# Optimization experiments

Measured on AMD Instinct MI355X. Metric: run time of the kernel, lower is better.

Reference implementation:

```python
import jax, jax.numpy as jnp
import numpy as np

N = 50000       # nodes
E = 800000      # edges (before self-loops)
F_IN = 128      # in_channels
HID = 32        # hidden_channels per head
HEADS = 4
OUT = 16        # out_channels
NEG_SLOPE = 0.2 # PyG GATConv leaky_relu slope
EPS = 1e-16     # PyG softmax denominator eps
BN_EPS = 1e-5


def setup_inputs() -> dict:
    key = jax.random.key(0)
    ks = jax.random.split(key, 20)
    rn = lambda k, shp, s=0.1: (jax.random.normal(k, shp, jnp.float32) * s)
    x = jax.random.normal(ks[0], (N, F_IN), jnp.float32)
    edge_index = jax.random.randint(ks[1], (2, E), 0, N, dtype=jnp.int32)
    D0 = HEADS * HID  # 128
    return {
        "x": x, "edge_index": edge_index,
        # layer 0: GATConv(F_IN -> HID, heads=HEADS, concat=True)
        "W0": rn(ks[2], (F_IN, HEADS * HID)), "as0": rn(ks[3], (HEADS, HID)),
        "ad0": rn(ks[4], (HEADS, HID)), "b0": jnp.zeros((D0,), jnp.float32),
        "g0": jnp.ones((D0,), jnp.float32) + rn(ks[5], (D0,), 0.05),
        "be0": rn(ks[6], (D0,), 0.05),
        # layer 1: GATConv(D0 -> HID, heads=HEADS, concat=True)
        "W1": rn(ks[7], (D0, HEADS * HID)), "as1": rn(ks[8], (HEADS, HID)),
        "ad1": rn(ks[9], (HEADS, HID)), "b1": jnp.zeros((D0,), jnp.float32),
        "g1": jnp.ones((D0,), jnp.float32) + rn(ks[10], (D0,), 0.05),
        "be1": rn(ks[11], (D0,), 0.05),
        # layer 2: GATConv(D0 -> OUT, heads=1, concat=False)
        "W2": rn(ks[12], (D0, OUT)), "as2": rn(ks[13], (1, OUT)),
        "ad2": rn(ks[14], (1, OUT)), "b2": jnp.zeros((OUT,), jnp.float32),
    }


def _gat(x, src, dst, W, a_s, a_d, b, heads, ch, concat):
    n = x.shape[0]
    h = (x @ W).reshape(n, heads, ch)                       # [N,H,C]
    score_s = (h * a_s).sum(-1)                             # [N,H]
    score_d = (h * a_d).sum(-1)                             # [N,H]
    e = jax.nn.leaky_relu(score_s[src] + score_d[dst], NEG_SLOPE)  # [E,H]
    emax = jax.ops.segment_max(e, dst, num_segments=n)
    emax = jnp.where(jnp.isfinite(emax), emax, 0.0)
    p = jnp.exp(e - emax[dst])
    denom = jax.ops.segment_sum(p, dst, num_segments=n)
    alpha = p / (denom[dst] + EPS)                          # segment softmax over dst
    out = jax.ops.segment_sum(h[src] * alpha[:, :, None], dst, num_segments=n)
    out = out.reshape(n, heads * ch) if concat else out.mean(axis=1)
    return out + b


def _bn(x, g, be):
    m = x.mean(0)
    v = x.var(0)
    return (x - m) * jax.lax.rsqrt(v + BN_EPS) * g + be


def reference(x, edge_index, W0, as0, ad0, b0, g0, be0,
              W1, as1, ad1, b1, g1, be1, W2, as2, ad2, b2):
    n = x.shape[0]
    loop = jnp.arange(n, dtype=edge_index.dtype)
    src = jnp.concatenate([edge_index[0], loop])  # PyG add_self_loops
    dst = jnp.concatenate([edge_index[1], loop])
    h = _gat(x, src, dst, W0, as0, ad0, b0, HEADS, HID, True)
    h = jax.nn.elu(_bn(h, g0, be0))                 # dropout disabled (eval)
    h = _gat(h, src, dst, W1, as1, ad1, b1, HEADS, HID, True)
    h = jax.nn.elu(_bn(h, g1, be1))
    return _gat(h, src, dst, W2, as2, ad2, b2, 1, OUT, False)
```

## Files before the change

kernel.cpp:

```cpp
#include <hip/hip_runtime.h>
#include <hip/hip_bf16.h>
#include <math.h>

#define NEG_SLOPE 0.2f
#define EPS_SM 1e-16f
#define BN_EPS 1e-5f
#define RANK_BLOCKS 512

typedef __attribute__((ext_vector_type(8))) short bf16x8;
typedef __attribute__((ext_vector_type(4))) float f32x4;

__device__ __forceinline__ float lrelu(float x) { return x > 0.f ? x : NEG_SLOPE * x; }
__device__ __forceinline__ ushort f2bf(float f) {
    uint u = __float_as_uint(f);
    return (ushort)((u + 0x7FFFu + ((u >> 16) & 1u)) >> 16);
}
__device__ __forceinline__ float bfl(uint u) { return __uint_as_float(u << 16); }
__device__ __forceinline__ float bfh(uint u) { return __uint_as_float(u & 0xFFFF0000u); }

__global__ void pack_w(const float* __restrict__ W0, const float* __restrict__ W1,
                       const float* __restrict__ W2, ushort* __restrict__ P0,
                       ushort* __restrict__ P1, ushort* __restrict__ P2) {
    int i = blockIdx.x * blockDim.x + threadIdx.x;
    const float* W;
    ushort* P;
    int NC, s;
    if (i < 16384) { W = W0; P = P0; NC = 128; s = i; }
    else if (i < 32768) { W = W1; P = P1; NC = 128; s = i - 16384; }
    else if (i < 34816) { W = W2; P = P2; NC = 16; s = i - 32768; }
    else return;
    int k = s / NC, col = s % NC;
    int CT = NC >> 4;
    int dst = (((k >> 5) * CT + (col >> 4)) << 9) +
              (((col & 15) | (((k >> 3) & 3) << 4)) << 3) + (k & 7);
    P[dst] = f2bf(W[s]);
}

template <int NC, int HEADS, bool XBN, bool RANKFUSE>
__global__ __launch_bounds__(256) void gemm_mfma(
    const void* __restrict__ Xv, const ushort* __restrict__ Wp, ushort* __restrict__ Hb,
    int n, const float* __restrict__ sumsP, const float* __restrict__ g,
    const float* __restrict__ be, const float* __restrict__ as_, const float* __restrict__ ad_,
    float* __restrict__ ss, float* __restrict__ sd,
    const int* __restrict__ dstE, int E, int* __restrict__ deg, ushort* __restrict__ rank) {
    int tid = threadIdx.x;
    if constexpr (RANKFUSE) {
        if ((int)blockIdx.x < RANK_BLOCKS) {
            int T = RANK_BLOCKS * 256;
            for (int i = (int)blockIdx.x * 256 + tid; i < E; i += T)
                rank[i] = (ushort)atomicAdd(&deg[dstE[i]], 1);
            return;
        }
    }
    constexpr int CT = NC / 16;
    constexpr int FPH = NC / HEADS / 16;
    __shared__ __align__(16) ushort Xb[64 * 128];
    __shared__ float ssl[64 * HEADS], sdl[64 * HEADS];
    int bid = RANKFUSE ? ((int)blockIdx.x - RANK_BLOCKS) : (int)blockIdx.x;
    int row0 = bid * 64;
    if constexpr (!XBN) {
        const float* X = (const float*)Xv;
#pragma unroll
        for (int i = 0; i < 8; ++i) {
            int idx = tid + i * 256;
            int row = idx >> 5, q = idx & 31;
            int gr = row0 + row;
            float4 v = make_float4(0.f, 0.f, 0.f, 0.f);
            if (gr < n) v = ((const float4*)(X + (long)gr * 128))[q];
            ushort4 p = make_ushort4(f2bf(v.x), f2bf(v.y), f2bf(v.z), f2bf(v.w));
            int s = (q >> 1) ^ (row & 15);
            *(ushort4*)&Xb[row * 128 + s * 8 + (q & 1) * 4] = p;
        }
    } else {
        const ushort* X = (const ushort*)Xv;
        int c8 = (tid & 15) * 8;
        float inv_n = 1.f / (float)n;
        float bm[8], bs[8], bb[8];
#pragma unroll
        for (int j = 0; j < 8; ++j) {
            int ch = c8 + j;
            float m = sumsP[ch * 16] * inv_n;
            float vv = fmaxf(sumsP[(128 + ch) * 16] * inv_n - m * m, 0.f);
            bm[j] = m;
            bs[j] = rsqrtf(vv + BN_EPS) * g[ch];
            bb[j] = be[ch];
        }
#pragma unroll
        for (int i = 0; i < 4; ++i) {
            int idx = tid + i * 256;
            int row = idx >> 4, g8 = idx & 15;
            int gr = row0 + row;
            uint4 v = make_uint4(0, 0, 0, 0);
            if (gr < n) v = ((const uint4*)(X + (long)gr * 128))[g8];
            float a, b;
#define BNE(comp, j0)                                                  \
    a = bfl(comp); b = bfh(comp);                                      \
    a = (a - bm[j0]) * bs[j0] + bb[j0]; a = a > 0.f ? a : expm1f(a);   \
    b = (b - bm[j0 + 1]) * bs[j0 + 1] + bb[j0 + 1];                    \
    b = b > 0.f ? b : expm1f(b);                                       \
    comp = (uint)f2bf(a) | ((uint)f2bf(b) << 16);
            BNE(v.x, 0) BNE(v.y, 2) BNE(v.z, 4) BNE(v.w, 6)
#undef BNE
            int s = g8 ^ (row & 15);
            *(uint4*)&Xb[row * 128 + s * 8] = v;
        }
    }
    __syncthreads();
    int lane = tid & 63;
    int w = tid >> 6;
    int r0 = w * 16;
    int lrow = lane & 15, lhi = lane >> 4;
    f32x4 zero = {0.f, 0.f, 0.f, 0.f};
    f32x4 acc[CT];
#pragma unroll
    for (int f = 0; f < CT; ++f) acc[f] = zero;
    const ushort* xr = &Xb[(r0 + lrow) * 128];
#pragma unroll
    for (int ks = 0; ks < 4; ++ks) {
        int kg = ks * 4 + lhi;
        bf16x8 a = *(const bf16x8*)&xr[(kg ^ lrow) << 3];
#pragma unroll
        for (int f = 0; f < CT; ++f) {
            bf16x8 b = *(const bf16x8*)&Wp[((ks * CT + f) * 64 + lane) * 8];
            acc[f] = __builtin_amdgcn_mfma_f32_16x16x32_bf16(a, b, acc[f], 0, 0, 0);
        }
    }
    __syncthreads();
#pragma unroll
    for (int f = 0; f < CT; ++f)
#pragma unroll
        for (int j = 0; j < 4; ++j)
            Xb[(r0 + lhi * 4 + j) * NC + f * 16 + lrow] = f2bf(acc[f][j]);
    float asv[CT], adv[CT];
#pragma unroll
    for (int f = 0; f < CT; ++f) {
        asv[f] = as_[f * 16 + lrow];
        adv[f] = ad_[f * 16 + lrow];
    }
#pragma unroll
    for (int h = 0; h < HEADS; ++h) {
        float ps[4] = {}, pd[4] = {};
#pragma unroll
        for (int fi = 0; fi < FPH; ++fi) {
            int f = h * FPH + fi;
#pragma unroll
            for (int j = 0; j < 4; ++j) {
                ps[j] = fmaf(acc[f][j], asv[f], ps[j]);
                pd[j] = fmaf(acc[f][j], adv[f], pd[j]);
            }
        }
#pragma unroll
        for (int j = 0; j < 4; ++j) {
#pragma unroll
            for (int d = 1; d < 16; d <<= 1) {
                ps[j] += __shfl_xor(ps[j], d, 64);
                pd[j] += __shfl_xor(pd[j], d, 64);
            }
            if (lrow == 0) {
                ssl[(r0 + lhi * 4 + j) * HEADS + h] = ps[j];
                sdl[(r0 + lhi * 4 + j) * HEADS + h] = pd[j];
            }
        }
    }
    __syncthreads();
    constexpr int NU = 64 * NC / 8;
#pragma unroll
    for (int i = 0; i < (NU + 255) / 256; ++i) {
        int idx = tid + i * 256;
        if (idx < NU) {
            int row = idx / (NC / 8), c8i = idx % (NC / 8);
            int gr = row0 + row;
            if (gr < n) ((uint4*)&Hb[(long)gr * NC])[c8i] = ((const uint4*)Xb)[idx];
        }
    }
    if (tid < 64 * HEADS) {
        int row = tid / HEADS, hh = tid % HEADS;
        int gr = row0 + row;
        if (gr < n) {
            ss[(long)gr * HEADS + hh] = ssl[tid];
            sd[(long)gr * HEADS + hh] = sdl[tid];
        }
    }
}

__global__ __launch_bounds__(1024) void scan_kernel(const int* __restrict__ deg,
                                                    int* __restrict__ offs, int n) {
    __shared__ int wsum[16];
    __shared__ int wpre[16];
    __shared__ int carry_s;
    int tid = threadIdx.x;
    int lane = tid & 63;
    int w = tid >> 6;
    if (tid == 0) carry_s = 0;
    __syncthreads();
    int nv = (n + 3) >> 2;
    for (int base = 0; base < nv; base += 1024) {
        int carry = carry_s;
        int gi = base + tid;
        int e0 = gi * 4;
        int4 v = make_int4(0, 0, 0, 0);
        if (e0 + 3 < n) {
            v = ((const int4*)deg)[gi];
        } else if (e0 < n) {
            v.x = deg[e0];
            if (e0 + 1 < n) v.y = deg[e0 + 1];
            if (e0 + 2 < n) v.z = deg[e0 + 2];
        }
        int tsum = v.x + v.y + v.z + v.w;
        int incl = tsum;
#pragma unroll
        for (int d = 1; d < 64; d <<= 1) {
            int t = __shfl_up(incl, d, 64);
            if (lane >= d) incl += t;
        }
        if (lane == 63) wsum[w] = incl;
        __syncthreads();
        if (w == 0 && lane < 16) {
            int s = wsum[lane];
#pragma unroll
            for (int d = 1; d < 16; d <<= 1) {
                int t = __shfl_up(s, d, 64);
                if (lane >= d) s += t;
            }
            wpre[lane] = s;
        }
        __syncthreads();
        int wbase = (w == 0) ? 0 : wpre[w - 1];
        int ex = carry + wbase + incl - tsum;
        if (e0 < n) {
            int4 o;
            o.x = ex;
            o.y = ex + v.x;
            o.z = o.y + v.y;
            o.w = o.z + v.z;
            if (e0 + 3 < n) {
                ((int4*)offs)[gi] = o;
            } else {
                offs[e0] = o.x;
                if (e0 + 1 < n) offs[e0 + 1] = o.y;
                if (e0 + 2 < n) offs[e0 + 2] = o.z;
            }
        }
        __syncthreads();
        if (tid == 1023) carry_s = carry + wpre[15];
        __syncthreads();
    }
}

__global__ void scatter_kernel(const int* __restrict__ src, const int* __restrict__ dst,
                               const ushort* __restrict__ rank, const int* __restrict__ offs,
                               int E, int* __restrict__ srcs) {
    int i = blockIdx.x * blockDim.x + threadIdx.x;
    int T = gridDim.x * blockDim.x;
    for (; i < E; i += T) {
        int d = dst[i];
        srcs[offs[d] + (int)rank[i]] = src[i];
    }
}

__global__ __launch_bounds__(256) void gat_gather4(
    const uint* __restrict__ hb, const float* __restrict__ ss, const float* __restrict__ sd,
    const int* __restrict__ offs, const int* __restrict__ deg, const int* __restrict__ srcs,
    const float* __restrict__ bias, ushort* __restrict__ outb, int n) {
    int wid = threadIdx.x >> 6;
    int lane = threadIdx.x & 63;
    int node = blockIdx.x * 4 + wid;
    if (node >= n) return;
    int off = offs[node];
    int dg = deg[node];
    int grp = lane >> 4;
    int ll = lane & 15;
    int hd = ll >> 2;
    float sdn = sd[node * 4 + hd];
    float es = lrelu(ss[node * 4 + hd] + sdn);
    const uint* hrow = hb + ll * 4;
    float acc[8] = {};
    float sm = 0.f;
#pragma unroll 2
    for (int i = grp; i < dg; i += 4) {
        int s = srcs[off + i];
        float w = __expf(lrelu(ss[s * 4 + hd] + sdn));
        sm += w;
        uint4 hv = *(const uint4*)(hrow + (long)s * 64);
        acc[0] = fmaf(w, bfl(hv.x), acc[0]);
        acc[1] = fmaf(w, bfh(hv.x), acc[1]);
        acc[2] = fmaf(w, bfl(hv.y), acc[2]);
        acc[3] = fmaf(w, bfh(hv.y), acc[3]);
        acc[4] = fmaf(w, bfl(hv.z), acc[4]);
        acc[5] = fmaf(w, bfh(hv.z), acc[5]);
        acc[6] = fmaf(w, bfl(hv.w), acc[6]);
        acc[7] = fmaf(w, bfh(hv.w), acc[7]);
    }
#pragma unroll
    for (int j = 0; j < 8; ++j) {
        acc[j] += __shfl_xor(acc[j], 16, 64);
        acc[j] += __shfl_xor(acc[j], 32, 64);
    }
    sm += __shfl_xor(sm, 16, 64);
    sm += __shfl_xor(sm, 32, 64);
    float wS = __expf(es);
    sm += wS;
    uint4 hvS = *(const uint4*)(hrow + (long)node * 64);
    acc[0] = fmaf(wS, bfl(hvS.x), acc[0]);
    acc[1] = fmaf(wS, bfh(hvS.x), acc[1]);
    acc[2] = fmaf(wS, bfl(hvS.y), acc[2]);
    acc[3] = fmaf(wS, bfh(hvS.y), acc[3]);
    acc[4] = fmaf(wS, bfl(hvS.z), acc[4]);
    acc[5] = fmaf(wS, bfh(hvS.z), acc[5]);
    acc[6] = fmaf(wS, bfl(hvS.w), acc[6]);
    acc[7] = fmaf(wS, bfh(hvS.w), acc[7]);
    float inv = 1.f / (sm + EPS_SM);
    if (grp == 0) {
        float4 bA = *(const float4*)&bias[ll * 8];
        float4 bB = *(const float4*)&bias[ll * 8 + 4];
        uint4 p;
        p.x = (uint)f2bf(acc[0] * inv + bA.x) | ((uint)f2bf(acc[1] * inv + bA.y) << 16);
        p.y = (uint)f2bf(acc[2] * inv + bA.z) | ((uint)f2bf(acc[3] * inv + bA.w) << 16);
        p.z = (uint)f2bf(acc[4] * inv + bB.x) | ((uint)f2bf(acc[5] * inv + bB.y) << 16);
        p.w = (uint)f2bf(acc[6] * inv + bB.z) | ((uint)f2bf(acc[7] * inv + bB.w) << 16);
        *(uint4*)&outb[(long)node * 128 + ll * 8] = p;
    }
}

__global__ __launch_bounds__(256) void gat_gather1(
    const uint* __restrict__ hb2, const float* __restrict__ ss, const float* __restrict__ sd,
    const int* __restrict__ offs, const int* __restrict__ deg, const int* __restrict__ srcs,
    const float* __restrict__ bias, float* __restrict__ out, int n) {
    int wid = threadIdx.x >> 6;
    int lane = threadIdx.x & 63;
    int node = blockIdx.x * 4 + wid;
    if (node >= n) return;
    int off = offs[node];
    int dg = deg[node];
    int grp = lane >> 3;
    int ll = lane & 7;
    float sdn = sd[node];
    float es = lrelu(ss[node] + sdn);
    float a0 = 0.f, a1 = 0.f, sm = 0.f;
#pragma unroll 2
    for (int i = grp; i < dg; i += 8) {
        int s = srcs[off + i];
        float w = __expf(lrelu(ss[s] + sdn));
        sm += w;
        uint hv = hb2[s * 8 + ll];
        a0 = fmaf(w, bfl(hv), a0);
        a1 = fmaf(w, bfh(hv), a1);
    }
#pragma unroll
    for (int d = 8; d <= 32; d <<= 1) {
        a0 += __shfl_xor(a0, d, 64);
        a1 += __shfl_xor(a1, d, 64);
        sm += __shfl_xor(sm, d, 64);
    }
    float wS = __expf(es);
    sm += wS;
    uint hvS = hb2[node * 8 + ll];
    a0 = fmaf(wS, bfl(hvS), a0);
    a1 = fmaf(wS, bfh(hvS), a1);
    float inv = 1.f / (sm + EPS_SM);
    if (grp == 0) {
        float2 o = make_float2(a0 * inv + bias[ll * 2], a1 * inv + bias[ll * 2 + 1]);
        *(float2*)&out[(long)node * 16 + ll * 2] = o;
    }
}

__global__ __launch_bounds__(256) void bn_stats_bf16(const uint4* __restrict__ X4,
                                                     float* __restrict__ sumsP, int n) {
    __shared__ float red[4096];
    int tid = threadIdx.x;
    float s[8] = {}, s2[8] = {};
    long tot = (long)n * 16;
    long T = (long)gridDim.x * 256;
    for (long i = (long)blockIdx.x * 256 + tid; i < tot; i += T) {
        uint4 v = X4[i];
        float f;
        f = bfl(v.x); s[0] += f; s2[0] = fmaf(f, f, s2[0]);
        f = bfh(v.x); s[1] += f; s2[1] = fmaf(f, f, s2[1]);
        f = bfl(v.y); s[2] += f; s2[2] = fmaf(f, f, s2[2]);
        f = bfh(v.y); s[3] += f; s2[3] = fmaf(f, f, s2[3]);
        f = bfl(v.z); s[4] += f; s2[4] = fmaf(f, f, s2[4]);
        f = bfh(v.z); s[5] += f; s2[5] = fmaf(f, f, s2[5]);
        f = bfl(v.w); s[6] += f; s2[6] = fmaf(f, f, s2[6]);
        f = bfh(v.w); s[7] += f; s2[7] = fmaf(f, f, s2[7]);
    }
#pragma unroll
    for (int j = 0; j < 8; ++j) {
        red[j * 256 + tid] = s[j];
        red[(8 + j) * 256 + tid] = s2[j];
    }
    __syncthreads();
    int ch = tid & 127, st = tid >> 7;
    int base = (st * 8 + (ch & 7)) * 256 + (ch >> 3);
    float a = 0.f;
#pragma unroll
    for (int rep = 0; rep < 16; ++rep) a += red[base + rep * 16];
    atomicAdd(&sumsP[tid * 16], a);
}

extern "C" void kernel_launch(void* const* d_in, const int* in_sizes, int n_in,
                              void* d_out, int out_size, void* d_ws, size_t ws_size,
                              hipStream_t stream) {
    const float* x = (const float*)d_in[0];
    const int* ei = (const int*)d_in[1];
    const float* W0 = (const float*)d_in[2];
    const float* as0 = (const float*)d_in[3];
    const float* ad0 = (const float*)d_in[4];
    const float* b0 = (const float*)d_in[5];
    const float* g0 = (const float*)d_in[6];
    const float* be0 = (const float*)d_in[7];
    const float* W1 = (const float*)d_in[8];
    const float* as1 = (const float*)d_in[9];
    const float* ad1 = (const float*)d_in[10];
    const float* b1 = (const float*)d_in[11];
    const float* g1 = (const float*)d_in[12];
    const float* be1 = (const float*)d_in[13];
    const float* W2 = (const float*)d_in[14];
    const float* as2 = (const float*)d_in[15];
    const float* ad2 = (const float*)d_in[16];
    const float* b2 = (const float*)d_in[17];

    int n = in_sizes[0] / 128;
    int E = in_sizes[1] / 2;
    const int* srcA = ei;
    const int* dstA = ei + E;

    char* base = (char*)d_ws;
    auto alloc = [&](size_t bytes) {
        char* p = base;
        base += (bytes + 255) & ~(size_t)255;
        return p;
    };
    ushort* hb = (ushort*)alloc((size_t)n * 128 * 2);
    ushort* actb = (ushort*)alloc((size_t)n * 128 * 2);
    ushort* h2b = (ushort*)alloc((size_t)n * 16 * 2);
    float* ssb = (float*)alloc((size_t)n * 4 * 4);
    float* sdb = (float*)alloc((size_t)n * 4 * 4);
    float* sumsP0 = (float*)alloc(4096 * 4);
    float* sumsP1 = (float*)alloc(4096 * 4);
    int* deg = (int*)alloc((size_t)n * 4);
    int* offs = (int*)alloc((size_t)n * 4);
    ushort* rank = (ushort*)alloc((size_t)E * 2);
    int* srcs = (int*)alloc((size_t)E * 4);
    ushort* Wp0 = (ushort*)alloc(16384 * 2);
    ushort* Wp1 = (ushort*)alloc(16384 * 2);
    ushort* Wp2 = (ushort*)alloc(2048 * 2);

    float* out = (float*)d_out;

    hipMemsetAsync(deg, 0, (size_t)n * 4, stream);
    hipMemsetAsync(sumsP0, 0, 4096 * 4 * 2, stream);

    pack_w<<<136, 256, 0, stream>>>(W0, W1, W2, Wp0, Wp1, Wp2);

    int gGemm = (n + 63) / 64;
    int gWave = (n + 3) / 4;

    gemm_mfma<128, 4, false, true><<<RANK_BLOCKS + gGemm, 256, 0, stream>>>(
        x, Wp0, hb, n, nullptr, g0, be0, as0, ad0, ssb, sdb, dstA, E, deg, rank);
    scan_kernel<<<1, 1024, 0, stream>>>(deg, offs, n);
    scatter_kernel<<<2048, 256, 0, stream>>>(srcA, dstA, rank, offs, E, srcs);

    gat_gather4<<<gWave, 256, 0, stream>>>((const uint*)hb, ssb, sdb, offs, deg, srcs, b0, actb, n);
    bn_stats_bf16<<<256, 256, 0, stream>>>((const uint4*)actb, sumsP0, n);

    gemm_mfma<128, 4, true, false><<<gGemm, 256, 0, stream>>>(
        actb, Wp1, hb, n, sumsP0, g0, be0, as1, ad1, ssb, sdb, nullptr, 0, nullptr, nullptr);
    gat_gather4<<<gWave, 256, 0, stream>>>((const uint*)hb, ssb, sdb, offs, deg, srcs, b1, actb, n);
    bn_stats_bf16<<<256, 256, 0, stream>>>((const uint4*)actb, sumsP1, n);

    gemm_mfma<16, 1, true, false><<<gGemm, 256, 0, stream>>>(
        actb, Wp2, h2b, n, sumsP1, g1, be1, as2, ad2, ssb, sdb, nullptr, 0, nullptr, nullptr);
    gat_gather1<<<gWave, 256, 0, stream>>>((const uint*)h2b, ssb, sdb, offs, deg, srcs, b2, out, n);
}
```

Baseline: 242.8 us.

## Pad degree counters to cache lines, unroll rank/scatter loops, derive degree from offsets

Each node's degree counter now sits in its own 64-byte slot, so the atomics that count degrees and assign ranks stop contending on shared cache lines. A small compact kernel then copies the counters into a dense array for the scan. The rank and scatter loops are unrolled four-way so more independent atomics and loads are in flight, and the rank block count is halved. The scan now writes offs[n], so the gather kernels compute degree as offs[node+1]-off instead of reading a separate array, at the cost of one extra kernel launch and a larger counter memset.

```diff
diff --git a/kernel.cpp b/kernel.cpp
--- a/kernel.cpp
+++ b/kernel.cpp
@@ -5,7 +5,7 @@
 #define NEG_SLOPE 0.2f
 #define EPS_SM 1e-16f
 #define BN_EPS 1e-5f
-#define RANK_BLOCKS 512
+#define RANK_BLOCKS 256
 
 typedef __attribute__((ext_vector_type(8))) short bf16x8;
 typedef __attribute__((ext_vector_type(4))) float f32x4;
@@ -42,13 +42,24 @@
     int n, const float* __restrict__ sumsP, const float* __restrict__ g,
     const float* __restrict__ be, const float* __restrict__ as_, const float* __restrict__ ad_,
     float* __restrict__ ss, float* __restrict__ sd,
-    const int* __restrict__ dstE, int E, int* __restrict__ deg, ushort* __restrict__ rank) {
+    const int* __restrict__ dstE, int E, int* __restrict__ degP, ushort* __restrict__ rank) {
     int tid = threadIdx.x;
     if constexpr (RANKFUSE) {
         if ((int)blockIdx.x < RANK_BLOCKS) {
-            int T = RANK_BLOCKS * 256;
-            for (int i = (int)blockIdx.x * 256 + tid; i < E; i += T)
-                rank[i] = (ushort)atomicAdd(&deg[dstE[i]], 1);
+            const int T = RANK_BLOCKS * 256;
+            int i = (int)blockIdx.x * 256 + tid;
+            for (; i + 3 * T < E; i += 4 * T) {
+                int d0 = dstE[i], d1 = dstE[i + T], d2 = dstE[i + 2 * T], d3 = dstE[i + 3 * T];
+                ushort r0 = (ushort)atomicAdd(&degP[d0 << 4], 1);
+                ushort r1 = (ushort)atomicAdd(&degP[d1 << 4], 1);
+                ushort r2 = (ushort)atomicAdd(&degP[d2 << 4], 1);
+                ushort r3 = (ushort)atomicAdd(&degP[d3 << 4], 1);
+                rank[i] = r0;
+                rank[i + T] = r1;
+                rank[i + 2 * T] = r2;
+                rank[i + 3 * T] = r3;
+            }
+            for (; i < E; i += T) rank[i] = (ushort)atomicAdd(&degP[dstE[i] << 4], 1);
             return;
         }
     }
@@ -181,6 +192,11 @@
             sd[(long)gr * HEADS + hh] = sdl[tid];
         }
     }
+}
+
+__global__ void compact_deg(const int* __restrict__ degP, int* __restrict__ deg, int n) {
+    int i = blockIdx.x * blockDim.x + threadIdx.x;
+    if (i < n) deg[i] = degP[i << 4];
 }
 
 __global__ __launch_bounds__(1024) void scan_kernel(const int* __restrict__ deg,
@@ -245,29 +261,38 @@
         if (tid == 1023) carry_s = carry + wpre[15];
         __syncthreads();
     }
+    if (tid == 0) offs[n] = carry_s;
 }
 
 __global__ void scatter_kernel(const int* __restrict__ src, const int* __restrict__ dst,
                                const ushort* __restrict__ rank, const int* __restrict__ offs,
                                int E, int* __restrict__ srcs) {
+    const int T = gridDim.x * blockDim.x;
     int i = blockIdx.x * blockDim.x + threadIdx.x;
-    int T = gridDim.x * blockDim.x;
-    for (; i < E; i += T) {
-        int d = dst[i];
-        srcs[offs[d] + (int)rank[i]] = src[i];
-    }
+    for (; i + 3 * T < E; i += 4 * T) {
+        int d0 = dst[i], d1 = dst[i + T], d2 = dst[i + 2 * T], d3 = dst[i + 3 * T];
+        int p0 = offs[d0] + (int)rank[i];
+        int p1 = offs[d1] + (int)rank[i + T];
+        int p2 = offs[d2] + (int)rank[i + 2 * T];
+        int p3 = offs[d3] + (int)rank[i + 3 * T];
+        srcs[p0] = src[i];
+        srcs[p1] = src[i + T];
+        srcs[p2] = src[i + 2 * T];
+        srcs[p3] = src[i + 3 * T];
+    }
+    for (; i < E; i += T) srcs[offs[dst[i]] + (int)rank[i]] = src[i];
 }
 
 __global__ __launch_bounds__(256) void gat_gather4(
     const uint* __restrict__ hb, const float* __restrict__ ss, const float* __restrict__ sd,
-    const int* __restrict__ offs, const int* __restrict__ deg, const int* __restrict__ srcs,
+    const int* __restrict__ offs, const int* __restrict__ srcs,
     const float* __restrict__ bias, ushort* __restrict__ outb, int n) {
     int wid = threadIdx.x >> 6;
     int lane = threadIdx.x & 63;
     int node = blockIdx.x * 4 + wid;
     if (node >= n) return;
     int off = offs[node];
-    int dg = deg[node];
+    int dg = offs[node + 1] - off;
     int grp = lane >> 4;
     int ll = lane & 15;
     int hd = ll >> 2;
@@ -324,14 +349,14 @@
 
 __global__ __launch_bounds__(256) void gat_gather1(
     const uint* __restrict__ hb2, const float* __restrict__ ss, const float* __restrict__ sd,
-    const int* __restrict__ offs, const int* __restrict__ deg, const int* __restrict__ srcs,
+    const int* __restrict__ offs, const int* __restrict__ srcs,
     const float* __restrict__ bias, float* __restrict__ out, int n) {
     int wid = threadIdx.x >> 6;
     int lane = threadIdx.x & 63;
     int node = blockIdx.x * 4 + wid;
     if (node >= n) return;
     int off = offs[node];
-    int dg = deg[node];
+    int dg = offs[node + 1] - off;
     int grp = lane >> 3;
     int ll = lane & 7;
     float sdn = sd[node];
@@ -437,8 +462,9 @@
     float* sdb = (float*)alloc((size_t)n * 4 * 4);
     float* sumsP0 = (float*)alloc(4096 * 4);
     float* sumsP1 = (float*)alloc(4096 * 4);
+    int* degP = (int*)alloc((size_t)n * 64);
     int* deg = (int*)alloc((size_t)n * 4);
-    int* offs = (int*)alloc((size_t)n * 4);
+    int* offs = (int*)alloc(((size_t)n + 1) * 4);
     ushort* rank = (ushort*)alloc((size_t)E * 2);
     int* srcs = (int*)alloc((size_t)E * 4);
     ushort* Wp0 = (ushort*)alloc(16384 * 2);
@@ -447,28 +473,30 @@
 
     float* out = (float*)d_out;
 
-    hipMemsetAsync(deg, 0, (size_t)n * 4, stream);
+    hipMemsetAsync(degP, 0, (size_t)n * 64, stream);
     hipMemsetAsync(sumsP0, 0, 4096 * 4 * 2, stream);
 
     pack_w<<<136, 256, 0, stream>>>(W0, W1, W2, Wp0, Wp1, Wp2);
 
     int gGemm = (n + 63) / 64;
     int gWave = (n + 3) / 4;
+    int gNode = (n + 255) / 256;
 
     gemm_mfma<128, 4, false, true><<<RANK_BLOCKS + gGemm, 256, 0, stream>>>(
-        x, Wp0, hb, n, nullptr, g0, be0, as0, ad0, ssb, sdb, dstA, E, deg, rank);
+        x, Wp0, hb, n, nullptr, g0, be0, as0, ad0, ssb, sdb, dstA, E, degP, rank);
+    compact_deg<<<gNode, 256, 0, stream>>>(degP, deg, n);
     scan_kernel<<<1, 1024, 0, stream>>>(deg, offs, n);
     scatter_kernel<<<2048, 256, 0, stream>>>(srcA, dstA, rank, offs, E, srcs);
 
-    gat_gather4<<<gWave, 256, 0, stream>>>((const uint*)hb, ssb, sdb, offs, deg, srcs, b0, actb, n);
+    gat_gather4<<<gWave, 256, 0, stream>>>((const uint*)hb, ssb, sdb, offs, srcs, b0, actb, n);
     bn_stats_bf16<<<256, 256, 0, stream>>>((const uint4*)actb, sumsP0, n);
 
     gemm_mfma<128, 4, true, false><<<gGemm, 256, 0, stream>>>(
         actb, Wp1, hb, n, sumsP0, g0, be0, as1, ad1, ssb, sdb, nullptr, 0, nullptr, nullptr);
-    gat_gather4<<<gWave, 256, 0, stream>>>((const uint*)hb, ssb, sdb, offs, deg, srcs, b1, actb, n);
+    gat_gather4<<<gWave, 256, 0, stream>>>((const uint*)hb, ssb, sdb, offs, srcs, b1, actb, n);
     bn_stats_bf16<<<256, 256, 0, stream>>>((const uint4*)actb, sumsP1, n);
 
     gemm_mfma<16, 1, true, false><<<gGemm, 256, 0, stream>>>(
         actb, Wp2, h2b, n, sumsP1, g1, be1, as2, ad2, ssb, sdb, nullptr, 0, nullptr, nullptr);
-    gat_gather1<<<gWave, 256, 0, stream>>>((const uint*)h2b, ssb, sdb, offs, deg, srcs, b2, out, n);
-}
+    gat_gather1<<<gWave, 256, 0, stream>>>((const uint*)h2b, ssb, sdb, offs, srcs, b2, out, n);
+}
```

Measured after the change: 240.0 us. About the same (-1.2%).
